# Optimization experiments

Hardware: AMD Instinct MI355X
Metric: run time of the kernel (lower is better)

Reference implementation:

```python
import jax, jax.numpy as jnp
import numpy as np
import math

EMBED_DIM = 1024
NUM_HEADS = 16
HEAD_DIM = EMBED_DIM // NUM_HEADS
DIFFUSION_STEPS = 2
ALPHA = 0.05
DETACH_P = True


def setup_inputs() -> dict:
    key = jax.random.key(0)
    ks = jax.random.split(key, 9)
    B, N, D = 1, 2048, EMBED_DIM
    s = 1.0 / math.sqrt(D)
    inp = {
        "hidden_states": jax.random.normal(ks[0], (B, N, D), dtype=jnp.float32),
        # torch nn.Linear weight is [out,in]; we store [in,out] so y = x @ W + b
        "Wq": jax.random.normal(ks[1], (D, D), dtype=jnp.float32) * s,
        "bq": jnp.zeros((D,), dtype=jnp.float32),
        "Wk": jax.random.normal(ks[2], (D, D), dtype=jnp.float32) * s,
        "bk": jnp.zeros((D,), dtype=jnp.float32),
        "Wv": jax.random.normal(ks[3], (D, D), dtype=jnp.float32) * s,
        "bv": jnp.zeros((D,), dtype=jnp.float32),
        "Wo": jax.random.normal(ks[4], (D, D), dtype=jnp.float32) * s,
        "bo": jnp.zeros((D,), dtype=jnp.float32),
    }
    return inp


def reference(hidden_states, Wq, bq, Wk, bk, Wv, bv, Wo, bo):
    B, N, D = hidden_states.shape
    H, hd = NUM_HEADS, HEAD_DIM

    def split_heads(x):  # [B,N,D] -> [B,H,N,hd]
        return x.reshape(B, N, H, hd).transpose(0, 2, 1, 3)

    Q = split_heads(hidden_states @ Wq + bq)
    K = split_heads(hidden_states @ Wk + bk)
    V = split_heads(hidden_states @ Wv + bv)

    # standard QK^T attention probabilities
    scores = jnp.einsum('bhqd,bhkd->bhqk', Q, K) / math.sqrt(hd)
    p0 = jax.nn.softmax(scores, axis=-1)

    # transition matrix from keys (note: scaled by sqrt(embed_dim), not head_dim)
    sim = jnp.einsum('bhid,bhjd->bhij', K, K) / math.sqrt(D)
    P = jax.nn.softmax(sim, axis=-1)
    if DETACH_P:
        P = jax.lax.stop_gradient(P)

    # iterative diffusion: p <- (1-alpha)*p0 + alpha * p @ P
    p = p0
    for _ in range(DIFFUSION_STEPS):
        p = (1.0 - ALPHA) * p0 + ALPHA * jnp.einsum('bhqn,bhnm->bhqm', p, P)

    attn = jnp.einsum('bhqk,bhkd->bhqd', p, V)          # [B,H,N,hd]
    attn = attn.transpose(0, 2, 1, 3).reshape(B, N, H * hd)
    out = attn @ Wo + bo
    return out, p
```

## Files before the change

kernel.cpp:

```cpp
#include <hip/hip_runtime.h>

#define N_TOK 2048
#define DMODEL 1024
#define NHEAD 16
#define HDIM 64

typedef __attribute__((ext_vector_type(8))) __bf16 bf16x8;
typedef __attribute__((ext_vector_type(4))) float f32x4;
typedef __attribute__((ext_vector_type(2))) long longx2;
typedef __attribute__((ext_vector_type(4))) int i32x4;
typedef __attribute__((ext_vector_type(8))) int i32x8;

__device__ __forceinline__ float bf2f(unsigned short h) {
  return __uint_as_float(((unsigned int)h) << 16);
}
__device__ __forceinline__ unsigned short f2bf(float f) {
  unsigned int u = __float_as_uint(f);
  unsigned int r = (u + 0x7fffu + ((u >> 16) & 1u)) >> 16;
  return (unsigned short)r;
}
__device__ __forceinline__ unsigned int pack4_fp8(float a, float b, float c, float d) {
  int v = __builtin_amdgcn_cvt_pk_fp8_f32(a, b, 0, false);
  v = __builtin_amdgcn_cvt_pk_fp8_f32(c, d, v, true);
  return (unsigned int)v;
}
__device__ __forceinline__ int swz8(int k8, int row) {
  return k8 ^ ((row & 7) << 4);
}

__device__ __forceinline__ void async16(const void* g, void* l) {
  __builtin_amdgcn_global_load_lds((__attribute__((address_space(1))) void*)(g),
                                   (__attribute__((address_space(3))) void*)(l),
                                   16, 0, 0);
}

#define FP8_SCALE 256.0f
#define FP8_INV2  (1.0f / (256.0f * 256.0f))

struct GemmP {
  const unsigned short* A;
  const unsigned short* B;
  const unsigned short* Eb;
  const float* bias;
  float* Cf;
  unsigned short* Cb;
  long long sA, sB, sE, sCf, sCb;
  int lda, ldb, ldE, ldCf, ldCb;
  int M, N, K;
  float alpha, beta;
};

__global__ __launch_bounds__(256) void gemm_bt_kernel(GemmP g) {
  __shared__ __attribute__((aligned(16))) unsigned short As[128 * 32];
  __shared__ __attribute__((aligned(16))) unsigned short Bs[128 * 32];
  const int tid = threadIdx.x;
  const int lane = tid & 63;
  const int wv = tid >> 6;
  const int wr = wv >> 1, wc = wv & 1;
  const long long z = blockIdx.z;
  const unsigned short* A = g.A + z * g.sA;
  const unsigned short* B = g.B + z * g.sB;
  const int tm = blockIdx.y * 128;
  const int tn = blockIdx.x * 128;

  const int r0 = tid >> 2;
  const int r1 = (tid + 256) >> 2;
  const int kof = (tid & 3) * 8;
  int bn0 = tn + r0; if (bn0 > g.N - 1) bn0 = g.N - 1;
  int bn1 = tn + r1; if (bn1 > g.N - 1) bn1 = g.N - 1;

  const unsigned short* pa0 = A + (long long)(tm + r0) * g.lda + kof;
  const unsigned short* pa1 = A + (long long)(tm + r1) * g.lda + kof;
  const unsigned short* pb0 = B + (long long)bn0 * g.ldb + kof;
  const unsigned short* pb1 = B + (long long)bn1 * g.ldb + kof;

  unsigned short* la0 = &As[tid * 8];
  unsigned short* la1 = &As[(tid + 256) * 8];
  unsigned short* lb0 = &Bs[tid * 8];
  unsigned short* lb1 = &Bs[(tid + 256) * 8];

  const int aroff = (wr * 64 + (lane & 15)) * 32 + (lane >> 4) * 8;
  const int broff = (wc * 64 + (lane & 15)) * 32 + (lane >> 4) * 8;

  f32x4 acc[4][4] = {};

  for (int kk = 0; kk < g.K; kk += 32) {
    __syncthreads();
    async16(pa0 + kk, la0);
    async16(pa1 + kk, la1);
    async16(pb0 + kk, lb0);
    async16(pb1 + kk, lb1);
    __syncthreads();
    bf16x8 af[4], bfr[4];
#pragma unroll
    for (int i = 0; i < 4; i++)
      af[i] = *(const bf16x8*)&As[aroff + i * 16 * 32];
#pragma unroll
    for (int j = 0; j < 4; j++)
      bfr[j] = *(const bf16x8*)&Bs[broff + j * 16 * 32];
#pragma unroll
    for (int i = 0; i < 4; i++)
#pragma unroll
      for (int j = 0; j < 4; j++)
        acc[i][j] = __builtin_amdgcn_mfma_f32_16x16x32_bf16(af[i], bfr[j], acc[i][j], 0, 0, 0);
  }

  const unsigned short* Eb = g.Eb ? g.Eb + z * g.sE : nullptr;
  float* Cf = g.Cf ? g.Cf + z * g.sCf : nullptr;
  unsigned short* Cb = g.Cb ? g.Cb + z * g.sCb : nullptr;
  const int cbase = tn + wc * 64 + (lane & 15);
  const int rbase = tm + wr * 64 + (lane >> 4) * 4;
#pragma unroll
  for (int i = 0; i < 4; i++) {
#pragma unroll
    for (int j = 0; j < 4; j++) {
      int col = cbase + j * 16;
      if (col < g.N) {
        float bs = g.bias ? g.bias[col] : 0.f;
#pragma unroll
        for (int r = 0; r < 4; r++) {
          int row = rbase + i * 16 + r;
          float v = g.alpha * acc[i][j][r] + bs;
          if (Eb) v += g.beta * bf2f(Eb[(long long)row * g.ldE + col]);
          if (Cf) Cf[(long long)row * g.ldCf + col] = v;
          if (Cb) Cb[(long long)row * g.ldCb + col] = f2bf(v);
        }
      }
    }
  }
}

struct Gemm8P {
  const unsigned char* A;
  const unsigned char* B;
  const unsigned short* Eb;
  float* Cf;
  unsigned short* Cb;
  long long sA, sB, sE, sCf, sCb;
  int lda, ldb, ldE, ldCf, ldCb;
  int K;
  float alpha, beta;
};

__global__ __launch_bounds__(256) void gemm_fp8_kernel(Gemm8P g) {
  __shared__ __attribute__((aligned(16))) unsigned char smem[65536];
  unsigned char* As0 = smem;
  unsigned char* Bs0 = smem + 32768;
  float* Cs = (float*)smem;
  const int tid = threadIdx.x;
  const int lane = tid & 63;
  const int wv = tid >> 6;
  const int wr = wv >> 1, wc = wv & 1;

  const unsigned int nx = gridDim.x, ny = gridDim.y;
  unsigned int orig = (blockIdx.z * ny + blockIdx.y) * nx + blockIdx.x;
  unsigned int nwg = nx * ny * gridDim.z;
  unsigned int wg = (orig & 7) * (nwg >> 3) + (orig >> 3);
  const int bx = wg % nx;
  unsigned int t1 = wg / nx;
  const int by = t1 % ny;
  const int bz = t1 / ny;

  const long long z = bz;
  const unsigned char* A = g.A + z * g.sA;
  const unsigned char* B = g.B + z * g.sB;
  const int tm = by * 128;
  const int tn = bx * 128;

  const int rs = tid >> 3;
  const int ks = (tid & 7) * 16;
  const unsigned char* pa0 = A + (long long)(tm + rs) * g.lda + ks;
  const unsigned char* pb0 = B + (long long)(tn + rs) * g.ldb + ks;
  const long long sa32 = 32LL * g.lda;
  const long long sb32 = 32LL * g.ldb;

  const int sw = (lane & 7) << 4;
  const int kg = (lane >> 4) * 32;
  const int klo = kg ^ sw;
  const int khi = (kg + 16) ^ sw;
  const int aoff0 = (wr * 64 + (lane & 15)) * 128;
  const int boff0 = (wc * 64 + (lane & 15)) * 128;

  f32x4 acc[4][4] = {};

  auto STAGE = [&](int buf, int kk) {
    unsigned char* la = As0 + buf * 16384 + tid * 16;
    unsigned char* lb = Bs0 + buf * 16384 + tid * 16;
    async16(pa0 + kk, la);
    async16(pa0 + sa32 + kk, la + 4096);
    async16(pa0 + 2 * sa32 + kk, la + 8192);
    async16(pa0 + 3 * sa32 + kk, la + 12288);
    async16(pb0 + kk, lb);
    async16(pb0 + sb32 + kk, lb + 4096);
    async16(pb0 + 2 * sb32 + kk, lb + 8192);
    async16(pb0 + 3 * sb32 + kk, lb + 12288);
  };

  auto COMPUTE = [&](int buf) {
    const unsigned char* ab = As0 + buf * 16384;
    const unsigned char* bb = Bs0 + buf * 16384;
    i32x8 a8[4], b8[4];
#pragma unroll
    for (int i = 0; i < 4; i++) {
      i32x4 lo = *(const i32x4*)(ab + aoff0 + i * 16 * 128 + klo);
      i32x4 hi = *(const i32x4*)(ab + aoff0 + i * 16 * 128 + khi);
      a8[i] = __builtin_shufflevector(lo, hi, 0, 1, 2, 3, 4, 5, 6, 7);
    }
#pragma unroll
    for (int j = 0; j < 4; j++) {
      i32x4 lo = *(const i32x4*)(bb + boff0 + j * 16 * 128 + klo);
      i32x4 hi = *(const i32x4*)(bb + boff0 + j * 16 * 128 + khi);
      b8[j] = __builtin_shufflevector(lo, hi, 0, 1, 2, 3, 4, 5, 6, 7);
    }
#pragma unroll
    for (int i = 0; i < 4; i++)
#pragma unroll
      for (int j = 0; j < 4; j++)
        acc[i][j] = __builtin_amdgcn_mfma_scale_f32_16x16x128_f8f6f4(
            a8[i], b8[j], acc[i][j], 0, 0, 0, 0x7f7f7f7f, 0, 0x7f7f7f7f);
  };

  const int NT = g.K >> 7;
  STAGE(0, 0);
  int cur = 0;
  for (int t = 0; t < NT - 1; ++t) {
    STAGE(cur ^ 1, (t + 1) << 7);
    asm volatile("s_waitcnt vmcnt(8)" ::: "memory");
    __builtin_amdgcn_s_barrier();
    __builtin_amdgcn_sched_barrier(0);
    COMPUTE(cur);
    __builtin_amdgcn_sched_barrier(0);
    __builtin_amdgcn_s_barrier();
    cur ^= 1;
  }
  asm volatile("s_waitcnt vmcnt(0)" ::: "memory");
  __builtin_amdgcn_s_barrier();
  __builtin_amdgcn_sched_barrier(0);
  COMPUTE(cur);

  __syncthreads();
  const int lrow0 = wr * 64 + (lane >> 4) * 4;
  const int lcol0 = wc * 64 + (lane & 15);
#pragma unroll
  for (int i = 0; i < 4; i++)
#pragma unroll
    for (int j = 0; j < 4; j++)
#pragma unroll
      for (int r = 0; r < 4; r++)
        Cs[(lrow0 + i * 16 + r) * 128 + lcol0 + j * 16] = acc[i][j][r];
  __syncthreads();

  const unsigned short* Eb = g.Eb + z * g.sE;
  float* Cf = g.Cf + z * g.sCf;
  unsigned short* Cb = g.Cb + z * g.sCb;
  const int rr = tid >> 5;
  const int c4 = (tid & 31) * 4;
#pragma unroll
  for (int p = 0; p < 16; p++) {
    int row = p * 8 + rr;
    f32x4 v = *(const f32x4*)&Cs[row * 128 + c4];
    long long gr = (long long)(tm + row);
    uint2 e = *(const uint2*)&Eb[gr * g.ldE + tn + c4];
    f32x4 o;
    o.x = g.alpha * v.x + g.beta * bf2f((unsigned short)(e.x & 0xffff));
    o.y = g.alpha * v.y + g.beta * bf2f((unsigned short)(e.x >> 16));
    o.z = g.alpha * v.z + g.beta * bf2f((unsigned short)(e.y & 0xffff));
    o.w = g.alpha * v.w + g.beta * bf2f((unsigned short)(e.y >> 16));
    *(f32x4*)&Cf[gr * g.ldCf + tn + c4] = o;
    uint2 ob;
    ob.x = (unsigned)f2bf(o.x) | ((unsigned)f2bf(o.y) << 16);
    ob.y = (unsigned)f2bf(o.z) | ((unsigned)f2bf(o.w) << 16);
    *(uint2*)&Cb[gr * g.ldCb + tn + c4] = ob;
  }
}

struct AttnP {
  const unsigned short* A;
  const unsigned short* B;
  float* Part;
  long long sA, sB;
  int lda, ldb, G;
};

__global__ __launch_bounds__(256) void attn_part_kernel(AttnP g) {
  __shared__ __attribute__((aligned(16))) unsigned short As[128 * 32];
  __shared__ __attribute__((aligned(16))) unsigned short Bs[64 * 32];
  const int tid = threadIdx.x;
  const int lane = tid & 63;
  const int w = tid >> 6;
  const int z = blockIdx.y;
  const int kz = blockIdx.z;
  const unsigned short* A = g.A + (long long)z * g.sA;
  const unsigned short* B = g.B + (long long)z * g.sB;
  const int tm = blockIdx.x * 128;
  const int k0 = kz * 512;

  const int rA0 = tid >> 2;
  const int rA1 = 64 + (tid >> 2);
  const int kof = (tid & 3) * 8;
  const unsigned short* pa0 = A + (long long)(tm + rA0) * g.lda + k0 + kof;
  const unsigned short* pa1 = A + (long long)(tm + rA1) * g.lda + k0 + kof;
  const unsigned short* pb0 = B + (long long)(tid >> 2) * g.ldb + k0 + kof;
  unsigned short* la0 = &As[tid * 8];
  unsigned short* la1 = &As[(tid + 256) * 8];
  unsigned short* lb0 = &Bs[tid * 8];

  const int aoff = (w * 32 + (lane & 15)) * 32 + (lane >> 4) * 8;
  const int boff = (lane & 15) * 32 + (lane >> 4) * 8;

  f32x4 acc[2][4] = {};

  for (int kk = 0; kk < 512; kk += 32) {
    __syncthreads();
    async16(pa0 + kk, la0);
    async16(pa1 + kk, la1);
    async16(pb0 + kk, lb0);
    __syncthreads();
    bf16x8 af[2], bfr[4];
#pragma unroll
    for (int i = 0; i < 2; i++)
      af[i] = *(const bf16x8*)&As[aoff + i * 16 * 32];
#pragma unroll
    for (int j = 0; j < 4; j++)
      bfr[j] = *(const bf16x8*)&Bs[boff + j * 16 * 32];
#pragma unroll
    for (int i = 0; i < 2; i++)
#pragma unroll
      for (int j = 0; j < 4; j++)
        acc[i][j] = __builtin_amdgcn_mfma_f32_16x16x32_bf16(af[i], bfr[j], acc[i][j], 0, 0, 0);
  }

  float* P = g.Part + ((long long)(kz * g.G + z) * N_TOK + tm) * 64;
#pragma unroll
  for (int i = 0; i < 2; i++) {
#pragma unroll
    for (int j = 0; j < 4; j++) {
      int col = (lane & 15) + j * 16;
#pragma unroll
      for (int r = 0; r < 4; r++) {
        int row = w * 32 + i * 16 + (lane >> 4) * 4 + r;
        P[(long long)row * 64 + col] = acc[i][j][r];
      }
    }
  }
}

__global__ __launch_bounds__(256) void attn_reduce_kernel(const float* Part, unsigned short* ATT,
                                                          int G, int h0) {
  int idx = blockIdx.x * 256 + threadIdx.x;
  int f = idx * 4;
  int z = f / (N_TOK * 64);
  int rem = f % (N_TOK * 64);
  int row = rem >> 6;
  int col = rem & 63;
  long long stride = (long long)G * N_TOK * 64;
  const float* p0 = Part + ((long long)z * N_TOK + row) * 64 + col;
  float4 s = *(const float4*)p0;
  float4 a = *(const float4*)(p0 + stride);
  float4 b = *(const float4*)(p0 + 2 * stride);
  float4 c = *(const float4*)(p0 + 3 * stride);
  s.x += a.x + b.x + c.x; s.y += a.y + b.y + c.y;
  s.z += a.z + b.z + c.z; s.w += a.w + b.w + c.w;
  uint2 o;
  o.x = (unsigned)f2bf(s.x) | ((unsigned)f2bf(s.y) << 16);
  o.y = (unsigned)f2bf(s.z) | ((unsigned)f2bf(s.w) << 16);
  *(uint2*)&ATT[(long long)row * DMODEL + (h0 + z) * 64 + col] = o;
}


__global__ __launch_bounds__(256) void cast_f32_bf16_kernel(const float* x, unsigned short* y) {
  int i = blockIdx.x * 256 + threadIdx.x;
  const float4* src = (const float4*)x;
  float4 a = src[i * 2], b = src[i * 2 + 1];
  uint4 o;
  o.x = (unsigned)f2bf(a.x) | ((unsigned)f2bf(a.y) << 16);
  o.y = (unsigned)f2bf(a.z) | ((unsigned)f2bf(a.w) << 16);
  o.z = (unsigned)f2bf(b.x) | ((unsigned)f2bf(b.y) << 16);
  o.w = (unsigned)f2bf(b.z) | ((unsigned)f2bf(b.w) << 16);
  ((uint4*)y)[i] = o;
}

__global__ __launch_bounds__(256) void transpose_w_kernel(const float* in, unsigned short* out,
                                                          int rows, int cols) {
  __shared__ float t[32][33];
  int c = blockIdx.x * 32 + threadIdx.x;
  int r0 = blockIdx.y * 32;
#pragma unroll
  for (int j = 0; j < 32; j += 8)
    t[threadIdx.y + j][threadIdx.x] = in[(long long)(r0 + threadIdx.y + j) * cols + c];
  __syncthreads();
  int r = r0 + threadIdx.x;
#pragma unroll
  for (int j = 0; j < 32; j += 8)
    out[(long long)(blockIdx.x * 32 + threadIdx.y + j) * rows + r] =
        f2bf(t[threadIdx.x][threadIdx.y + j]);
}

__global__ __launch_bounds__(256) void transpose_bf_kernel(const unsigned short* in,
                                                           unsigned short* out,
                                                           int rows, int cols) {
  __shared__ unsigned short t[32][34];
  int c = blockIdx.x * 32 + threadIdx.x;
  int r0 = blockIdx.y * 32;
#pragma unroll
  for (int j = 0; j < 32; j += 8)
    t[threadIdx.y + j][threadIdx.x] = in[(long long)(r0 + threadIdx.y + j) * cols + c];
  __syncthreads();
  int r = r0 + threadIdx.x;
#pragma unroll
  for (int j = 0; j < 32; j += 8)
    out[(long long)(blockIdx.x * 32 + threadIdx.y + j) * rows + r] = t[threadIdx.x][threadIdx.y + j];
}

__global__ __launch_bounds__(256) void softmax_rows_kernel(const float* S, unsigned short* P,
                                                           unsigned char* P8, float scale) {
  __shared__ float redm[4];
  __shared__ float reds[4];
  long long row = blockIdx.x;
  const float4* src = (const float4*)(S + row * 2048);
  float4 A = src[threadIdx.x * 2], B = src[threadIdx.x * 2 + 1];
  float v[8] = {A.x, A.y, A.z, A.w, B.x, B.y, B.z, B.w};
#pragma unroll
  for (int i = 0; i < 8; i++) v[i] *= scale;
  float m = v[0];
#pragma unroll
  for (int i = 1; i < 8; i++) m = fmaxf(m, v[i]);
#pragma unroll
  for (int o = 32; o > 0; o >>= 1) m = fmaxf(m, __shfl_xor(m, o));
  if ((threadIdx.x & 63) == 0) redm[threadIdx.x >> 6] = m;
  __syncthreads();
  m = fmaxf(fmaxf(redm[0], redm[1]), fmaxf(redm[2], redm[3]));
  float e[8];
  float s = 0.f;
#pragma unroll
  for (int i = 0; i < 8; i++) { e[i] = __expf(v[i] - m); s += e[i]; }
#pragma unroll
  for (int o = 32; o > 0; o >>= 1) s += __shfl_xor(s, o);
  if ((threadIdx.x & 63) == 0) reds[threadIdx.x >> 6] = s;
  __syncthreads();
  s = (reds[0] + reds[1]) + (reds[2] + reds[3]);
  float inv = 1.f / s;
  float p[8];
#pragma unroll
  for (int i = 0; i < 8; i++) p[i] = e[i] * inv;
  uint4 o4;
  o4.x = (unsigned)f2bf(p[0]) | ((unsigned)f2bf(p[1]) << 16);
  o4.y = (unsigned)f2bf(p[2]) | ((unsigned)f2bf(p[3]) << 16);
  o4.z = (unsigned)f2bf(p[4]) | ((unsigned)f2bf(p[5]) << 16);
  o4.w = (unsigned)f2bf(p[6]) | ((unsigned)f2bf(p[7]) << 16);
  ((uint4*)(P + row * 2048))[threadIdx.x] = o4;
  uint2 q;
  q.x = pack4_fp8(p[0] * FP8_SCALE, p[1] * FP8_SCALE, p[2] * FP8_SCALE, p[3] * FP8_SCALE);
  q.y = pack4_fp8(p[4] * FP8_SCALE, p[5] * FP8_SCALE, p[6] * FP8_SCALE, p[7] * FP8_SCALE);
  *(uint2*)(P8 + row * 2048 + swz8((int)threadIdx.x * 8, (int)row)) = q;
}

__global__ __launch_bounds__(256) void rowstats_bf_kernel(const unsigned short* S, float* mx,
                                                          float* rz, float scale) {
  __shared__ float redm[4];
  __shared__ float reds[4];
  long long row = blockIdx.x;
  uint4 raw = ((const uint4*)(S + row * 2048))[threadIdx.x];
  unsigned int w[4] = {raw.x, raw.y, raw.z, raw.w};
  float v[8];
#pragma unroll
  for (int i = 0; i < 4; i++) {
    v[2 * i] = bf2f((unsigned short)(w[i] & 0xffff)) * scale;
    v[2 * i + 1] = bf2f((unsigned short)(w[i] >> 16)) * scale;
  }
  float m = v[0];
#pragma unroll
  for (int i = 1; i < 8; i++) m = fmaxf(m, v[i]);
#pragma unroll
  for (int o = 32; o > 0; o >>= 1) m = fmaxf(m, __shfl_xor(m, o));
  if ((threadIdx.x & 63) == 0) redm[threadIdx.x >> 6] = m;
  __syncthreads();
  m = fmaxf(fmaxf(redm[0], redm[1]), fmaxf(redm[2], redm[3]));
  float s = 0.f;
#pragma unroll
  for (int i = 0; i < 8; i++) s += __expf(v[i] - m);
#pragma unroll
  for (int o = 32; o > 0; o >>= 1) s += __shfl_xor(s, o);
  if ((threadIdx.x & 63) == 0) reds[threadIdx.x >> 6] = s;
  __syncthreads();
  if (threadIdx.x == 0) {
    s = (reds[0] + reds[1]) + (reds[2] + reds[3]);
    mx[row] = m;
    rz[row] = 1.f / s;
  }
}

__global__ __launch_bounds__(256) void build_pt_kernel(const unsigned short* S, const float* mx,
                                                       const float* rz, unsigned char* PT,
                                                       float scale) {
  long long z = blockIdx.y;
  long long m = blockIdx.x;
  uint4 raw = ((const uint4*)(S + (z * 2048 + m) * 2048))[threadIdx.x];
  unsigned int w[4] = {raw.x, raw.y, raw.z, raw.w};
  float v[8];
#pragma unroll
  for (int i = 0; i < 4; i++) {
    v[2 * i] = bf2f((unsigned short)(w[i] & 0xffff)) * scale;
    v[2 * i + 1] = bf2f((unsigned short)(w[i] >> 16)) * scale;
  }
  const float4* mx4 = (const float4*)(mx + z * 2048);
  const float4* rz4 = (const float4*)(rz + z * 2048);
  float4 ma = mx4[threadIdx.x * 2], mb = mx4[threadIdx.x * 2 + 1];
  float4 ra = rz4[threadIdx.x * 2], rb = rz4[threadIdx.x * 2 + 1];
  float p[8];
  p[0] = __expf(v[0] - ma.x) * ra.x * FP8_SCALE;
  p[1] = __expf(v[1] - ma.y) * ra.y * FP8_SCALE;
  p[2] = __expf(v[2] - ma.z) * ra.z * FP8_SCALE;
  p[3] = __expf(v[3] - ma.w) * ra.w * FP8_SCALE;
  p[4] = __expf(v[4] - mb.x) * rb.x * FP8_SCALE;
  p[5] = __expf(v[5] - mb.y) * rb.y * FP8_SCALE;
  p[6] = __expf(v[6] - mb.z) * rb.z * FP8_SCALE;
  p[7] = __expf(v[7] - mb.w) * rb.w * FP8_SCALE;
  uint2 q;
  q.x = pack4_fp8(p[0], p[1], p[2], p[3]);
  q.y = pack4_fp8(p[4], p[5], p[6], p[7]);
  *(uint2*)(PT + (z * 2048 + m) * 2048 + swz8((int)threadIdx.x * 8, (int)m)) = q;
}


extern "C" void kernel_launch(void* const* d_in, const int* in_sizes, int n_in,
                              void* d_out, int out_size, void* d_ws, size_t ws_size,
                              hipStream_t stream) {
  const float* hs = (const float*)d_in[0];
  const float* Wq = (const float*)d_in[1];
  const float* bq = (const float*)d_in[2];
  const float* Wk = (const float*)d_in[3];
  const float* bk = (const float*)d_in[4];
  const float* Wv = (const float*)d_in[5];
  const float* bv = (const float*)d_in[6];
  const float* Wo = (const float*)d_in[7];
  const float* bo = (const float*)d_in[8];
  float* out = (float*)d_out;
  float* outp = out + (size_t)N_TOK * DMODEL;

  char* base = (char*)d_ws;
  size_t off = 0;
  auto alloc = [&](size_t bytes) -> void* {
    void* p = base + off;
    off += (bytes + 255) & ~(size_t)255;
    return p;
  };
  const size_t ND2 = (size_t)N_TOK * DMODEL * 2;
  unsigned short* Xbf = (unsigned short*)alloc(ND2);
  unsigned short* Qbf = (unsigned short*)alloc(ND2);
  unsigned short* Kbf = (unsigned short*)alloc(ND2);
  unsigned short* Vbf = (unsigned short*)alloc(ND2);
  unsigned short* Vt  = (unsigned short*)alloc(ND2);
  unsigned short* ATT = (unsigned short*)alloc(ND2);
  unsigned short* WT  = (unsigned short*)alloc((size_t)DMODEL * DMODEL * 2);
  float* mx = (float*)alloc((size_t)NHEAD * N_TOK * 4);
  float* rz = (float*)alloc((size_t)NHEAD * N_TOK * 4);
  float* Part = (float*)alloc((size_t)4 * NHEAD * N_TOK * 64 * 4);
  size_t fixed = off;

  const size_t SZ = (size_t)N_TOK * N_TOK;
  int G = 16;
  while (G > 1 && fixed + (size_t)G * SZ * 8 > ws_size) G >>= 1;
  float* SB           = (float*)alloc((size_t)G * SZ * 4);
  unsigned short* P0  = (unsigned short*)alloc((size_t)G * SZ * 2);
  unsigned char* P0q  = (unsigned char*)alloc((size_t)G * SZ);
  unsigned char* PT   = (unsigned char*)alloc((size_t)G * SZ);
  unsigned short* SIMB = (unsigned short*)SB;
  unsigned short* PB   = (unsigned short*)SB + G * SZ;

  auto gemm = [&](const GemmP& p, int nt, int mt, int batch) {
    gemm_bt_kernel<<<dim3(nt, mt, batch), 256, 0, stream>>>(p);
  };

  cast_f32_bf16_kernel<<<(N_TOK * DMODEL / 8) / 256, 256, 0, stream>>>(hs, Xbf);

  auto proj = [&](const float* W, const float* bias, unsigned short* dst) {
    transpose_w_kernel<<<dim3(32, 32), dim3(32, 8), 0, stream>>>(W, WT, DMODEL, DMODEL);
    GemmP p = {};
    p.A = Xbf; p.lda = DMODEL;
    p.B = WT;  p.ldb = DMODEL;
    p.bias = bias;
    p.Cb = dst; p.ldCb = DMODEL;
    p.M = N_TOK; p.N = DMODEL; p.K = DMODEL;
    p.alpha = 1.f;
    gemm(p, DMODEL / 128, N_TOK / 128, 1);
  };
  proj(Wq, bq, Qbf);
  proj(Wk, bk, Kbf);
  proj(Wv, bv, Vbf);
  transpose_bf_kernel<<<dim3(DMODEL / 32, N_TOK / 32), dim3(32, 8), 0, stream>>>(Vbf, Vt, N_TOK, DMODEL);

  const float sc_hd = 0.125f;
  const float sc_d  = 0.03125f;
  const float alpha = 0.05f;

  int ngroups = NHEAD / G;
  for (int gi = 0; gi < ngroups; gi++) {
    int h0 = gi * G;

    GemmP ps = {};
    ps.A = Qbf + h0 * HDIM; ps.sA = HDIM; ps.lda = DMODEL;
    ps.B = Kbf + h0 * HDIM; ps.sB = HDIM; ps.ldb = DMODEL;
    ps.Cf = SB; ps.sCf = (long long)SZ; ps.ldCf = N_TOK;
    ps.M = N_TOK; ps.N = N_TOK; ps.K = HDIM;
    ps.alpha = 1.f;
    gemm(ps, 16, 16, G);
    softmax_rows_kernel<<<G * N_TOK, 256, 0, stream>>>(SB, P0, P0q, sc_hd);

    GemmP pk = ps;
    pk.A = Kbf + h0 * HDIM;
    pk.Cf = nullptr;
    pk.Cb = SIMB; pk.sCb = (long long)SZ; pk.ldCb = N_TOK;
    gemm(pk, 16, 16, G);
    rowstats_bf_kernel<<<G * N_TOK, 256, 0, stream>>>(SIMB, mx, rz, sc_d);
    build_pt_kernel<<<dim3(N_TOK, G), 256, 0, stream>>>(SIMB, mx, rz, PT, sc_d);

    Gemm8P g8 = {};
    g8.A = P0q; g8.sA = (long long)SZ; g8.lda = N_TOK;
    g8.B = PT;  g8.sB = (long long)SZ; g8.ldb = N_TOK;
    g8.Eb = P0; g8.sE = (long long)SZ; g8.ldE = N_TOK;
    g8.Cf = outp + (size_t)h0 * SZ; g8.sCf = (long long)SZ; g8.ldCf = N_TOK;
    g8.Cb = PB; g8.sCb = (long long)SZ; g8.ldCb = N_TOK;
    g8.K = N_TOK;
    g8.alpha = alpha * FP8_INV2;
    g8.beta = 1.f - alpha;
    gemm_fp8_kernel<<<dim3(16, 16, G), 256, 0, stream>>>(g8);

    AttnP pa = {};
    pa.A = PB; pa.sA = (long long)SZ; pa.lda = N_TOK;
    pa.B = Vt + (size_t)h0 * HDIM * N_TOK; pa.sB = (long long)HDIM * N_TOK; pa.ldb = N_TOK;
    pa.Part = Part; pa.G = G;
    attn_part_kernel<<<dim3(16, G, 4), 256, 0, stream>>>(pa);
    attn_reduce_kernel<<<G * 128, 256, 0, stream>>>(Part, ATT, G, h0);
  }

  transpose_w_kernel<<<dim3(32, 32), dim3(32, 8), 0, stream>>>(Wo, WT, DMODEL, DMODEL);
  GemmP po = {};
  po.A = ATT; po.lda = DMODEL;
  po.B = WT;  po.ldb = DMODEL;
  po.bias = bo;
  po.Cf = out; po.ldCf = DMODEL;
  po.M = N_TOK; po.N = DMODEL; po.K = DMODEL;
  po.alpha = 1.f;
  gemm(po, DMODEL / 128, N_TOK / 128, 1);
}
```

Before: 1.027 ms.

## Fuse QK and KK score GEMMs with softmax via two-pass recompute kernels

Replaces the score GEMMs that wrote full fp32 and bf16 score matrices, plus the separate softmax, rowstats and build_pt passes, with two fused kernels. A stats kernel computes online row max and sum-exp per query tile. An emit kernel then recomputes the tiles and writes normalized bf16 and fp8 probabilities directly, using column statistics for the symmetric K·K transition matrix. This removes large round trips of score matrices through global memory at the cost of recomputing the cheap K=64 products twice. The emit kernel needs about 112KB of LDS and uses a strided shared-memory staging layout, which limits occupancy to a single block per CU.

```diff
diff --git a/kernel.cpp b/kernel.cpp
--- a/kernel.cpp
+++ b/kernel.cpp
@@ -7,7 +7,6 @@
 
 typedef __attribute__((ext_vector_type(8))) __bf16 bf16x8;
 typedef __attribute__((ext_vector_type(4))) float f32x4;
-typedef __attribute__((ext_vector_type(2))) long longx2;
 typedef __attribute__((ext_vector_type(4))) int i32x4;
 typedef __attribute__((ext_vector_type(8))) int i32x8;
 
@@ -127,6 +126,294 @@
         }
       }
     }
+  }
+}
+
+struct QKP {
+  const unsigned short* A;
+  const unsigned short* B;
+  float* mx;
+  float* rz;
+  unsigned short* Pbf;
+  unsigned char* P8;
+  float scale;
+  int colstats;
+};
+
+__global__ __launch_bounds__(256) void qk_stats_kernel(QKP g) {
+  __shared__ __attribute__((aligned(16))) unsigned short Qs[128 * 64];
+  __shared__ __attribute__((aligned(16))) unsigned short Ks[2][128 * 64];
+  __shared__ float redA[2][128];
+  __shared__ float redB[2][128];
+  const int tid = threadIdx.x;
+  const int lane = tid & 63;
+  const int wv = tid >> 6;
+  const int wr = wv >> 1, wc = wv & 1;
+  const int z = blockIdx.y;
+  const int tm = blockIdx.x * 128;
+  const unsigned short* A = g.A + z * HDIM;
+  const unsigned short* B = g.B + z * HDIM;
+
+  int sr[4], so[4];
+#pragma unroll
+  for (int k = 0; k < 4; k++) {
+    int c = tid + k * 256;
+    int row = c >> 3;
+    sr[k] = row;
+    so[k] = ((c & 7) ^ (row & 7)) * 8;
+  }
+#pragma unroll
+  for (int k = 0; k < 4; k++)
+    async16(A + (long long)(tm + sr[k]) * DMODEL + so[k], (char*)Qs + tid * 16 + k * 4096);
+#pragma unroll
+  for (int k = 0; k < 4; k++)
+    async16(B + (long long)sr[k] * DMODEL + so[k], (char*)Ks[0] + tid * 16 + k * 4096);
+  asm volatile("s_waitcnt vmcnt(0)" ::: "memory");
+  __builtin_amdgcn_s_barrier();
+
+  const int fr = lane & 15;
+  const int fg = lane >> 4;
+  bf16x8 qf[4][2];
+#pragma unroll
+  for (int i = 0; i < 4; i++)
+#pragma unroll
+    for (int s = 0; s < 2; s++) {
+      int r = wr * 64 + fr + i * 16;
+      int gl = (fg + s * 4) ^ (r & 7);
+      qf[i][s] = *(const bf16x8*)&Qs[r * 64 + gl * 8];
+    }
+
+  float m_[16], s_[16], mn_[16], t_[16];
+#pragma unroll
+  for (int q = 0; q < 16; q++) { m_[q] = -3.0e38f; s_[q] = 0.f; }
+
+  int buf = 0;
+  for (int kb = 0; kb < 16; kb++) {
+    f32x4 acc[4][4] = {};
+#pragma unroll
+    for (int j = 0; j < 4; j++) {
+      int r = wc * 64 + fr + j * 16;
+#pragma unroll
+      for (int s = 0; s < 2; s++) {
+        int gl = (fg + s * 4) ^ (r & 7);
+        bf16x8 bf = *(const bf16x8*)&Ks[buf][r * 64 + gl * 8];
+#pragma unroll
+        for (int i = 0; i < 4; i++)
+          acc[i][j] = __builtin_amdgcn_mfma_f32_16x16x32_bf16(qf[i][s], bf, acc[i][j], 0, 0, 0);
+      }
+    }
+    if (kb < 15) {
+#pragma unroll
+      for (int k = 0; k < 4; k++)
+        async16(B + (long long)((kb + 1) * 128 + sr[k]) * DMODEL + so[k],
+                (char*)Ks[buf ^ 1] + tid * 16 + k * 4096);
+    }
+#pragma unroll
+    for (int i = 0; i < 4; i++)
+#pragma unroll
+      for (int r = 0; r < 4; r++) {
+        float mm = fmaxf(fmaxf(acc[i][0][r], acc[i][1][r]),
+                         fmaxf(acc[i][2][r], acc[i][3][r]));
+        mn_[i * 4 + r] = mm * g.scale;
+      }
+#pragma unroll
+    for (int q = 0; q < 16; q++) {
+      float v = mn_[q];
+      v = fmaxf(v, __shfl_xor(v, 1));
+      v = fmaxf(v, __shfl_xor(v, 2));
+      v = fmaxf(v, __shfl_xor(v, 4));
+      v = fmaxf(v, __shfl_xor(v, 8));
+      mn_[q] = v;
+    }
+    if (fr == 0) {
+#pragma unroll
+      for (int i = 0; i < 4; i++)
+#pragma unroll
+        for (int r = 0; r < 4; r++)
+          redA[wc][wr * 64 + i * 16 + fg * 4 + r] = mn_[i * 4 + r];
+    }
+    __builtin_amdgcn_s_barrier();
+#pragma unroll
+    for (int i = 0; i < 4; i++)
+#pragma unroll
+      for (int r = 0; r < 4; r++) {
+        int row = wr * 64 + i * 16 + fg * 4 + r;
+        int q = i * 4 + r;
+        float mn = fmaxf(m_[q], fmaxf(redA[0][row], redA[1][row]));
+        float e0 = __expf(acc[i][0][r] * g.scale - mn);
+        float e1 = __expf(acc[i][1][r] * g.scale - mn);
+        float e2 = __expf(acc[i][2][r] * g.scale - mn);
+        float e3 = __expf(acc[i][3][r] * g.scale - mn);
+        t_[q] = (e0 + e1) + (e2 + e3);
+        mn_[q] = mn;
+      }
+#pragma unroll
+    for (int q = 0; q < 16; q++) {
+      float v = t_[q];
+      v += __shfl_xor(v, 1);
+      v += __shfl_xor(v, 2);
+      v += __shfl_xor(v, 4);
+      v += __shfl_xor(v, 8);
+      t_[q] = v;
+    }
+    if (fr == 0) {
+#pragma unroll
+      for (int i = 0; i < 4; i++)
+#pragma unroll
+        for (int r = 0; r < 4; r++)
+          redB[wc][wr * 64 + i * 16 + fg * 4 + r] = t_[i * 4 + r];
+    }
+    __builtin_amdgcn_s_barrier();
+#pragma unroll
+    for (int i = 0; i < 4; i++)
+#pragma unroll
+      for (int r = 0; r < 4; r++) {
+        int row = wr * 64 + i * 16 + fg * 4 + r;
+        int q = i * 4 + r;
+        float tt = redB[0][row] + redB[1][row];
+        s_[q] = s_[q] * __expf(m_[q] - mn_[q]) + tt;
+        m_[q] = mn_[q];
+      }
+    if (kb < 15) asm volatile("s_waitcnt vmcnt(0)" ::: "memory");
+    __builtin_amdgcn_s_barrier();
+    buf ^= 1;
+  }
+
+  if (fr == 0 && wc == 0) {
+#pragma unroll
+    for (int i = 0; i < 4; i++)
+#pragma unroll
+      for (int r = 0; r < 4; r++) {
+        int row = wr * 64 + i * 16 + fg * 4 + r;
+        int q = i * 4 + r;
+        g.mx[(long long)z * N_TOK + tm + row] = m_[q];
+        g.rz[(long long)z * N_TOK + tm + row] = 1.f / s_[q];
+      }
+  }
+}
+
+__global__ __launch_bounds__(256) void qk_emit_kernel(QKP g) {
+  __shared__ __attribute__((aligned(16))) unsigned short Qs[128 * 64];
+  __shared__ __attribute__((aligned(16))) unsigned short Ks[2][128 * 64];
+  __shared__ __attribute__((aligned(16))) float Ps[128 * 128];
+  const int tid = threadIdx.x;
+  const int lane = tid & 63;
+  const int wv = tid >> 6;
+  const int wr = wv >> 1, wc = wv & 1;
+  const int z = blockIdx.y;
+  const int tm = blockIdx.x * 128;
+  const unsigned short* A = g.A + z * HDIM;
+  const unsigned short* B = g.B + z * HDIM;
+
+  int sr[4], so[4];
+#pragma unroll
+  for (int k = 0; k < 4; k++) {
+    int c = tid + k * 256;
+    int row = c >> 3;
+    sr[k] = row;
+    so[k] = ((c & 7) ^ (row & 7)) * 8;
+  }
+#pragma unroll
+  for (int k = 0; k < 4; k++)
+    async16(A + (long long)(tm + sr[k]) * DMODEL + so[k], (char*)Qs + tid * 16 + k * 4096);
+#pragma unroll
+  for (int k = 0; k < 4; k++)
+    async16(B + (long long)sr[k] * DMODEL + so[k], (char*)Ks[0] + tid * 16 + k * 4096);
+  asm volatile("s_waitcnt vmcnt(0)" ::: "memory");
+  __builtin_amdgcn_s_barrier();
+
+  const int fr = lane & 15;
+  const int fg = lane >> 4;
+  bf16x8 qf[4][2];
+#pragma unroll
+  for (int i = 0; i < 4; i++)
+#pragma unroll
+    for (int s = 0; s < 2; s++) {
+      int r = wr * 64 + fr + i * 16;
+      int gl = (fg + s * 4) ^ (r & 7);
+      qf[i][s] = *(const bf16x8*)&Qs[r * 64 + gl * 8];
+    }
+
+  const int rr = tid >> 5;
+  const int c4 = (tid & 31) * 4;
+  const long long zn = (long long)z * N_TOK;
+  float mr_[16], rr_[16];
+  if (!g.colstats) {
+#pragma unroll
+    for (int p = 0; p < 16; p++) {
+      mr_[p] = g.mx[zn + tm + p * 8 + rr];
+      rr_[p] = g.rz[zn + tm + p * 8 + rr];
+    }
+  }
+
+  int buf = 0;
+  for (int kb = 0; kb < 16; kb++) {
+    f32x4 acc[4][4] = {};
+#pragma unroll
+    for (int j = 0; j < 4; j++) {
+      int r = wc * 64 + fr + j * 16;
+#pragma unroll
+      for (int s = 0; s < 2; s++) {
+        int gl = (fg + s * 4) ^ (r & 7);
+        bf16x8 bf = *(const bf16x8*)&Ks[buf][r * 64 + gl * 8];
+#pragma unroll
+        for (int i = 0; i < 4; i++)
+          acc[i][j] = __builtin_amdgcn_mfma_f32_16x16x32_bf16(qf[i][s], bf, acc[i][j], 0, 0, 0);
+      }
+    }
+#pragma unroll
+    for (int i = 0; i < 4; i++)
+#pragma unroll
+      for (int j = 0; j < 4; j++)
+#pragma unroll
+        for (int r = 0; r < 4; r++)
+          Ps[(wr * 64 + i * 16 + fg * 4 + r) * 128 + wc * 64 + fr + j * 16] =
+              acc[i][j][r] * g.scale;
+    __builtin_amdgcn_s_barrier();
+    if (kb < 15) {
+#pragma unroll
+      for (int k = 0; k < 4; k++)
+        async16(B + (long long)((kb + 1) * 128 + sr[k]) * DMODEL + so[k],
+                (char*)Ks[buf ^ 1] + tid * 16 + k * 4096);
+    }
+    const int ct = kb * 128;
+    float ma[4], ra[4];
+    if (g.colstats) {
+      float4 m4 = *(const float4*)&g.mx[zn + ct + c4];
+      float4 r4 = *(const float4*)&g.rz[zn + ct + c4];
+      ma[0] = m4.x; ma[1] = m4.y; ma[2] = m4.z; ma[3] = m4.w;
+      ra[0] = r4.x; ra[1] = r4.y; ra[2] = r4.z; ra[3] = r4.w;
+    }
+#pragma unroll
+    for (int p = 0; p < 16; p++) {
+      int row = p * 8 + rr;
+      f32x4 v = *(const f32x4*)&Ps[row * 128 + c4];
+      float pr[4];
+      if (g.colstats) {
+        pr[0] = __expf(v.x - ma[0]) * ra[0];
+        pr[1] = __expf(v.y - ma[1]) * ra[1];
+        pr[2] = __expf(v.z - ma[2]) * ra[2];
+        pr[3] = __expf(v.w - ma[3]) * ra[3];
+      } else {
+        pr[0] = __expf(v.x - mr_[p]) * rr_[p];
+        pr[1] = __expf(v.y - mr_[p]) * rr_[p];
+        pr[2] = __expf(v.z - mr_[p]) * rr_[p];
+        pr[3] = __expf(v.w - mr_[p]) * rr_[p];
+      }
+      long long prow = (zn + tm + row) * N_TOK;
+      if (g.Pbf) {
+        uint2 ob;
+        ob.x = (unsigned)f2bf(pr[0]) | ((unsigned)f2bf(pr[1]) << 16);
+        ob.y = (unsigned)f2bf(pr[2]) | ((unsigned)f2bf(pr[3]) << 16);
+        *(uint2*)&g.Pbf[prow + ct + c4] = ob;
+      }
+      unsigned o8 = pack4_fp8(pr[0] * FP8_SCALE, pr[1] * FP8_SCALE,
+                              pr[2] * FP8_SCALE, pr[3] * FP8_SCALE);
+      *(unsigned*)&g.P8[prow + ((ct + c4) ^ ((row & 7) << 4))] = o8;
+    }
+    if (kb < 15) asm volatile("s_waitcnt vmcnt(0)" ::: "memory");
+    __builtin_amdgcn_s_barrier();
+    buf ^= 1;
   }
 }
 
@@ -412,116 +699,6 @@
     out[(long long)(blockIdx.x * 32 + threadIdx.y + j) * rows + r] = t[threadIdx.x][threadIdx.y + j];
 }
 
-__global__ __launch_bounds__(256) void softmax_rows_kernel(const float* S, unsigned short* P,
-                                                           unsigned char* P8, float scale) {
-  __shared__ float redm[4];
-  __shared__ float reds[4];
-  long long row = blockIdx.x;
-  const float4* src = (const float4*)(S + row * 2048);
-  float4 A = src[threadIdx.x * 2], B = src[threadIdx.x * 2 + 1];
-  float v[8] = {A.x, A.y, A.z, A.w, B.x, B.y, B.z, B.w};
-#pragma unroll
-  for (int i = 0; i < 8; i++) v[i] *= scale;
-  float m = v[0];
-#pragma unroll
-  for (int i = 1; i < 8; i++) m = fmaxf(m, v[i]);
-#pragma unroll
-  for (int o = 32; o > 0; o >>= 1) m = fmaxf(m, __shfl_xor(m, o));
-  if ((threadIdx.x & 63) == 0) redm[threadIdx.x >> 6] = m;
-  __syncthreads();
-  m = fmaxf(fmaxf(redm[0], redm[1]), fmaxf(redm[2], redm[3]));
-  float e[8];
-  float s = 0.f;
-#pragma unroll
-  for (int i = 0; i < 8; i++) { e[i] = __expf(v[i] - m); s += e[i]; }
-#pragma unroll
-  for (int o = 32; o > 0; o >>= 1) s += __shfl_xor(s, o);
-  if ((threadIdx.x & 63) == 0) reds[threadIdx.x >> 6] = s;
-  __syncthreads();
-  s = (reds[0] + reds[1]) + (reds[2] + reds[3]);
-  float inv = 1.f / s;
-  float p[8];
-#pragma unroll
-  for (int i = 0; i < 8; i++) p[i] = e[i] * inv;
-  uint4 o4;
-  o4.x = (unsigned)f2bf(p[0]) | ((unsigned)f2bf(p[1]) << 16);
-  o4.y = (unsigned)f2bf(p[2]) | ((unsigned)f2bf(p[3]) << 16);
-  o4.z = (unsigned)f2bf(p[4]) | ((unsigned)f2bf(p[5]) << 16);
-  o4.w = (unsigned)f2bf(p[6]) | ((unsigned)f2bf(p[7]) << 16);
-  ((uint4*)(P + row * 2048))[threadIdx.x] = o4;
-  uint2 q;
-  q.x = pack4_fp8(p[0] * FP8_SCALE, p[1] * FP8_SCALE, p[2] * FP8_SCALE, p[3] * FP8_SCALE);
-  q.y = pack4_fp8(p[4] * FP8_SCALE, p[5] * FP8_SCALE, p[6] * FP8_SCALE, p[7] * FP8_SCALE);
-  *(uint2*)(P8 + row * 2048 + swz8((int)threadIdx.x * 8, (int)row)) = q;
-}
-
-__global__ __launch_bounds__(256) void rowstats_bf_kernel(const unsigned short* S, float* mx,
-                                                          float* rz, float scale) {
-  __shared__ float redm[4];
-  __shared__ float reds[4];
-  long long row = blockIdx.x;
-  uint4 raw = ((const uint4*)(S + row * 2048))[threadIdx.x];
-  unsigned int w[4] = {raw.x, raw.y, raw.z, raw.w};
-  float v[8];
-#pragma unroll
-  for (int i = 0; i < 4; i++) {
-    v[2 * i] = bf2f((unsigned short)(w[i] & 0xffff)) * scale;
-    v[2 * i + 1] = bf2f((unsigned short)(w[i] >> 16)) * scale;
-  }
-  float m = v[0];
-#pragma unroll
-  for (int i = 1; i < 8; i++) m = fmaxf(m, v[i]);
-#pragma unroll
-  for (int o = 32; o > 0; o >>= 1) m = fmaxf(m, __shfl_xor(m, o));
-  if ((threadIdx.x & 63) == 0) redm[threadIdx.x >> 6] = m;
-  __syncthreads();
-  m = fmaxf(fmaxf(redm[0], redm[1]), fmaxf(redm[2], redm[3]));
-  float s = 0.f;
-#pragma unroll
-  for (int i = 0; i < 8; i++) s += __expf(v[i] - m);
-#pragma unroll
-  for (int o = 32; o > 0; o >>= 1) s += __shfl_xor(s, o);
-  if ((threadIdx.x & 63) == 0) reds[threadIdx.x >> 6] = s;
-  __syncthreads();
-  if (threadIdx.x == 0) {
-    s = (reds[0] + reds[1]) + (reds[2] + reds[3]);
-    mx[row] = m;
-    rz[row] = 1.f / s;
-  }
-}
-
-__global__ __launch_bounds__(256) void build_pt_kernel(const unsigned short* S, const float* mx,
-                                                       const float* rz, unsigned char* PT,
-                                                       float scale) {
-  long long z = blockIdx.y;
-  long long m = blockIdx.x;
-  uint4 raw = ((const uint4*)(S + (z * 2048 + m) * 2048))[threadIdx.x];
-  unsigned int w[4] = {raw.x, raw.y, raw.z, raw.w};
-  float v[8];
-#pragma unroll
-  for (int i = 0; i < 4; i++) {
-    v[2 * i] = bf2f((unsigned short)(w[i] & 0xffff)) * scale;
-    v[2 * i + 1] = bf2f((unsigned short)(w[i] >> 16)) * scale;
-  }
-  const float4* mx4 = (const float4*)(mx + z * 2048);
-  const float4* rz4 = (const float4*)(rz + z * 2048);
-  float4 ma = mx4[threadIdx.x * 2], mb = mx4[threadIdx.x * 2 + 1];
-  float4 ra = rz4[threadIdx.x * 2], rb = rz4[threadIdx.x * 2 + 1];
-  float p[8];
-  p[0] = __expf(v[0] - ma.x) * ra.x * FP8_SCALE;
-  p[1] = __expf(v[1] - ma.y) * ra.y * FP8_SCALE;
-  p[2] = __expf(v[2] - ma.z) * ra.z * FP8_SCALE;
-  p[3] = __expf(v[3] - ma.w) * ra.w * FP8_SCALE;
-  p[4] = __expf(v[4] - mb.x) * rb.x * FP8_SCALE;
-  p[5] = __expf(v[5] - mb.y) * rb.y * FP8_SCALE;
-  p[6] = __expf(v[6] - mb.z) * rb.z * FP8_SCALE;
-  p[7] = __expf(v[7] - mb.w) * rb.w * FP8_SCALE;
-  uint2 q;
-  q.x = pack4_fp8(p[0], p[1], p[2], p[3]);
-  q.y = pack4_fp8(p[4], p[5], p[6], p[7]);
-  *(uint2*)(PT + (z * 2048 + m) * 2048 + swz8((int)threadIdx.x * 8, (int)m)) = q;
-}
-
 
 extern "C" void kernel_launch(void* const* d_in, const int* in_sizes, int n_in,
                               void* d_out, int out_size, void* d_ws, size_t ws_size,
@@ -555,6 +732,8 @@
   unsigned short* WT  = (unsigned short*)alloc((size_t)DMODEL * DMODEL * 2);
   float* mx = (float*)alloc((size_t)NHEAD * N_TOK * 4);
   float* rz = (float*)alloc((size_t)NHEAD * N_TOK * 4);
+  float* mxq = (float*)alloc((size_t)NHEAD * N_TOK * 4);
+  float* rzq = (float*)alloc((size_t)NHEAD * N_TOK * 4);
   float* Part = (float*)alloc((size_t)4 * NHEAD * N_TOK * 64 * 4);
   size_t fixed = off;
 
@@ -565,7 +744,6 @@
   unsigned short* P0  = (unsigned short*)alloc((size_t)G * SZ * 2);
   unsigned char* P0q  = (unsigned char*)alloc((size_t)G * SZ);
   unsigned char* PT   = (unsigned char*)alloc((size_t)G * SZ);
-  unsigned short* SIMB = (unsigned short*)SB;
   unsigned short* PB   = (unsigned short*)SB + G * SZ;
 
   auto gemm = [&](const GemmP& p, int nt, int mt, int batch) {
@@ -598,22 +776,19 @@
   for (int gi = 0; gi < ngroups; gi++) {
     int h0 = gi * G;
 
-    GemmP ps = {};
-    ps.A = Qbf + h0 * HDIM; ps.sA = HDIM; ps.lda = DMODEL;
-    ps.B = Kbf + h0 * HDIM; ps.sB = HDIM; ps.ldb = DMODEL;
-    ps.Cf = SB; ps.sCf = (long long)SZ; ps.ldCf = N_TOK;
-    ps.M = N_TOK; ps.N = N_TOK; ps.K = HDIM;
-    ps.alpha = 1.f;
-    gemm(ps, 16, 16, G);
-    softmax_rows_kernel<<<G * N_TOK, 256, 0, stream>>>(SB, P0, P0q, sc_hd);
-
-    GemmP pk = ps;
-    pk.A = Kbf + h0 * HDIM;
-    pk.Cf = nullptr;
-    pk.Cb = SIMB; pk.sCb = (long long)SZ; pk.ldCb = N_TOK;
-    gemm(pk, 16, 16, G);
-    rowstats_bf_kernel<<<G * N_TOK, 256, 0, stream>>>(SIMB, mx, rz, sc_d);
-    build_pt_kernel<<<dim3(N_TOK, G), 256, 0, stream>>>(SIMB, mx, rz, PT, sc_d);
+    QKP qp = {};
+    qp.A = Qbf + h0 * HDIM; qp.B = Kbf + h0 * HDIM;
+    qp.mx = mxq; qp.rz = rzq; qp.scale = sc_hd; qp.colstats = 0;
+    qk_stats_kernel<<<dim3(16, G), 256, 0, stream>>>(qp);
+    qp.Pbf = P0; qp.P8 = P0q;
+    qk_emit_kernel<<<dim3(16, G), 256, 0, stream>>>(qp);
+
+    QKP sp = {};
+    sp.A = Kbf + h0 * HDIM; sp.B = Kbf + h0 * HDIM;
+    sp.mx = mx; sp.rz = rz; sp.scale = sc_d; sp.colstats = 1;
+    qk_stats_kernel<<<dim3(16, G), 256, 0, stream>>>(sp);
+    sp.Pbf = nullptr; sp.P8 = PT;
+    qk_emit_kernel<<<dim3(16, G), 256, 0, stream>>>(sp);
 
     Gemm8P g8 = {};
     g8.A = P0q; g8.sA = (long long)SZ; g8.lda = N_TOK;
```

Measured after the change: 963.6 us. 1.07x faster.
